# Kernel optimization log

Hardware: AMD Instinct MI355X
Metric: run time of the kernel (lower is better)

Reference implementation:

```python
import jax, jax.numpy as jnp
import numpy as np

N_NODES = 20000
N_EDGES = 150000
IN_C = 512
OUT_C = 512
K_INIT = 7  # weight has K_INIT+1 = 8 slices, all used by the forward loop


def setup_inputs() -> dict:
    key = jax.random.key(0)
    k1, k2, k3, k4 = jax.random.split(key, 4)
    x = jax.random.normal(k1, (N_NODES, IN_C), dtype=jnp.float32)
    edge_index = jax.random.randint(k2, (2, N_EDGES), 0, N_NODES, dtype=jnp.int32)
    # uniform init as in reset_parameters: bound = 1/sqrt(in_channels * (K+1))
    bound = 1.0 / np.sqrt(IN_C * (K_INIT + 1))
    weight = jax.random.uniform(k3, (K_INIT + 1, IN_C, OUT_C), dtype=jnp.float32,
                                minval=-bound, maxval=bound)
    bias = jax.random.uniform(k4, (OUT_C,), dtype=jnp.float32,
                              minval=-bound, maxval=bound)
    return {"x": x, "edge_index": edge_index, "weight": weight, "bias": bias}


def _spmm(row, col, lap, x, num_nodes):
    # out[i] = sum_{e: row[e]==i} lap[e] * x[col[e]]
    msgs = lap[:, None] * x[col]  # [E, C] gather + scale
    return jax.ops.segment_sum(msgs, row, num_segments=num_nodes)


def reference(x, edge_index, weight, bias):
    row, col = edge_index[0], edge_index[1]
    num_nodes = x.shape[0]
    Kw = weight.shape[0]
    # degree^{-1/2} normalization of implicit adjacency, edge_attr = ones
    deg = jax.ops.segment_sum(jnp.ones_like(row, dtype=x.dtype), row,
                              num_segments=num_nodes)
    dinv = jnp.where(deg > 0, jax.lax.rsqrt(jnp.maximum(deg, 1e-30)), 0.0)
    lap = -dinv[row] * dinv[col]  # [E]
    Tx_0 = x
    out = Tx_0 @ weight[0]
    Tx_1 = _spmm(row, col, lap, x, num_nodes)
    out = out + Tx_1 @ weight[1]
    for k in range(2, Kw):
        Tx_2 = 2.0 * _spmm(row, col, lap, Tx_1, num_nodes) - Tx_0
        out = out + Tx_2 @ weight[k]
        Tx_0, Tx_1 = Tx_1, Tx_2
    return out + bias
```

## Files before the change

### kernel.cpp

```cpp
#include <hip/hip_runtime.h>

#define NN 20000
#define NP 20096
#define NE 150000
#define CC 512
#define KW 8
#define KT 4096
#define SCB 20

typedef __attribute__((ext_vector_type(8))) short short8;
typedef __attribute__((ext_vector_type(4))) float f32x4;
typedef __attribute__((ext_vector_type(4))) unsigned short ushort4v;
typedef __attribute__((ext_vector_type(8))) unsigned short ushort8v;

__device__ inline unsigned short f2bf(float f) {
  unsigned u = __builtin_bit_cast(unsigned, f);
  u += 0x7fffu + ((u >> 16) & 1u);
  return (unsigned short)(u >> 16);
}

__device__ inline float bf2f(unsigned short u) {
  return __builtin_bit_cast(float, (unsigned)u << 16);
}

__device__ inline void gload_lds16(const void* g, void* l) {
  __builtin_amdgcn_global_load_lds(
      (const __attribute__((address_space(1))) unsigned int*)g,
      (__attribute__((address_space(3))) unsigned int*)l, 16, 0, 0);
}


__global__ __launch_bounds__(256) void k_zero(int* __restrict__ deg, int* __restrict__ cursor) {
  int i = blockIdx.x * blockDim.x + threadIdx.x;
  if (i < NN) { deg[i] = 0; cursor[i] = 0; }
}

__global__ __launch_bounds__(256) void k_count(const int* __restrict__ row, int* __restrict__ deg) {
  int e = blockIdx.x * blockDim.x + threadIdx.x;
  if (e < NE) atomicAdd(&deg[row[e]], 1);
}

__global__ __launch_bounds__(256) void k_dinv(const int* __restrict__ deg, float* __restrict__ dinv) {
  int i = blockIdx.x * blockDim.x + threadIdx.x;
  if (i < NN) {
    int d = deg[i];
    dinv[i] = (d > 0) ? rsqrtf((float)d) : 0.0f;
  }
}

__global__ __launch_bounds__(1024) void k_scanA(const int* __restrict__ deg,
    int* __restrict__ row_off, int* __restrict__ bsum) {
  __shared__ int sm[1024];
  const int b = blockIdx.x, tid = threadIdx.x;
  int i = b * 1024 + tid;
  int v = (i < NN) ? deg[i] : 0;
  sm[tid] = v;
  __syncthreads();
  #pragma unroll
  for (int off = 1; off < 1024; off <<= 1) {
    int t = (tid >= off) ? sm[tid - off] : 0;
    __syncthreads();
    if (tid >= off) sm[tid] += t;
    __syncthreads();
  }
  if (i < NN) row_off[i] = sm[tid] - v;
  if (tid == 1023) bsum[b] = sm[1023];
}

__global__ __launch_bounds__(64) void k_scanB(int* __restrict__ bsum) {
  if (threadIdx.x == 0) {
    int run = 0;
    for (int b = 0; b < SCB; ++b) { int t = bsum[b]; bsum[b] = run; run += t; }
  }
}

__global__ __launch_bounds__(1024) void k_scanC(int* __restrict__ row_off, const int* __restrict__ bsum) {
  int i = blockIdx.x * 1024 + threadIdx.x;
  if (i < NN) row_off[i] += bsum[blockIdx.x];
  if (i == NN - 1) row_off[NN] = NE;
}

__global__ __launch_bounds__(256) void k_fill(const int* __restrict__ row, const int* __restrict__ col,
    const int* __restrict__ row_off, int* __restrict__ cursor, const float* __restrict__ dinv,
    int* __restrict__ csr_col, float* __restrict__ csr_val) {
  int e = blockIdx.x * blockDim.x + threadIdx.x;
  if (e < NE) {
    int r = row[e], c = col[e];
    int pos = row_off[r] + atomicAdd(&cursor[r], 1);
    csr_col[pos] = c;
    csr_val[pos] = -dinv[r] * dinv[c];
  }
}


__global__ __launch_bounds__(256) void k_wcast(const float* __restrict__ W, unsigned short* __restrict__ Bt) {
  __shared__ float sm[64][68];
  const int t = blockIdx.x;
  const int s = t >> 6;
  const int rem = t & 63;
  const int kt0 = (rem >> 3) * 64;
  const int nt0 = (rem & 7) * 64;
  const float* w = W + ((size_t)s << 18);
  const int tid = threadIdx.x;
  #pragma unroll
  for (int i = 0; i < 4; ++i) {
    int f = tid + i * 256;
    int r = f >> 4;
    int c4 = f & 15;
    float4 v = *(const float4*)&w[(size_t)(kt0 + r) * CC + nt0 + c4 * 4];
    sm[r][c4 * 4 + 0] = v.x; sm[r][c4 * 4 + 1] = v.y;
    sm[r][c4 * 4 + 2] = v.z; sm[r][c4 * 4 + 3] = v.w;
  }
  __syncthreads();
  #pragma unroll
  for (int i = 0; i < 2; ++i) {
    int g = tid + i * 256;
    int nl = g >> 3;
    int k8 = (g & 7) * 8;
    ushort8v o;
    #pragma unroll
    for (int j = 0; j < 8; ++j) o[j] = f2bf(sm[k8 + j][nl]);
    *(ushort8v*)&Bt[(size_t)(nt0 + nl) * KT + s * CC + kt0 + k8] = o;
  }
}

__global__ __launch_bounds__(256) void k_xcast(const float* __restrict__ x, unsigned short* __restrict__ txall) {
  size_t t = (size_t)blockIdx.x * 256 + threadIdx.x;
  size_t idx = t * 8;
  if (idx >= (size_t)NN * CC) return;
  size_t r = idx >> 9;
  int c = (int)(idx & 511);
  const float4* p = (const float4*)&x[idx];
  float4 a = p[0], b = p[1];
  ushort8v v;
  v[0] = f2bf(a.x); v[1] = f2bf(a.y); v[2] = f2bf(a.z); v[3] = f2bf(a.w);
  v[4] = f2bf(b.x); v[5] = f2bf(b.y); v[6] = f2bf(b.z); v[7] = f2bf(b.w);
  *(ushort8v*)&txall[r * KT + c] = v;
}


__global__ __launch_bounds__(256) void k_spmm(const unsigned short* __restrict__ gsrc,
    const unsigned short* __restrict__ gprev, unsigned short* __restrict__ gdst,
    const int* __restrict__ row_off, const int* __restrict__ csr_col,
    const float* __restrict__ csr_val, float alpha, float beta)
{
  const int tid = threadIdx.x;
  const int i = blockIdx.x * 4 + (tid >> 6);
  const int c8 = (tid & 63) * 8;
  const int e0 = row_off[i];
  const int e1 = row_off[i + 1];

  float acc[8] = {};
  for (int base = e0; base < e1; base += 8) {
    int   idxs[8];
    float vals[8];
    #pragma unroll
    for (int q = 0; q < 8; ++q) {
      int ee = base + q;
      bool ok = ee < e1;
      int ec = ok ? ee : (e1 - 1);
      idxs[q] = csr_col[ec];
      vals[q] = ok ? csr_val[ec] : 0.0f;
    }
    ushort8v xs[8];
    #pragma unroll
    for (int q = 0; q < 8; ++q)
      xs[q] = *(const ushort8v*)&gsrc[(size_t)idxs[q] * KT + c8];
    #pragma unroll
    for (int q = 0; q < 8; ++q)
      #pragma unroll
      for (int p = 0; p < 8; ++p)
        acc[p] += vals[q] * bf2f(xs[q][p]);
  }

  ushort8v bv;
  if (beta != 0.0f) {
    const ushort8v p = *(const ushort8v*)&gprev[(size_t)i * KT + c8];
    #pragma unroll
    for (int q = 0; q < 8; ++q)
      bv[q] = f2bf(alpha * acc[q] + beta * bf2f(p[q]));
  } else {
    #pragma unroll
    for (int q = 0; q < 8; ++q)
      bv[q] = f2bf(alpha * acc[q]);
  }
  *(ushort8v*)&gdst[(size_t)i * KT + c8] = bv;
}


__global__ __launch_bounds__(512) void k_gemm(const unsigned short* __restrict__ A,
    const unsigned short* __restrict__ Bt, float* __restrict__ C,
    const float* __restrict__ bias)
{
  __shared__ unsigned short smA[128 * 32];
  __shared__ unsigned short smB[128 * 32];
  const int tid  = threadIdx.x;
  const int lane = tid & 63;
  const int wave = tid >> 6;
  const int wr = wave >> 2;
  const int wc = wave & 3;

  const int nwg = (NP / 128) * 4;
  int bid = blockIdx.x;
  int q = nwg >> 3, rr = nwg & 7;
  int xcd = bid & 7, lid = bid >> 3;
  int wgid = (xcd < rr ? xcd * (q + 1) : rr * (q + 1) + (xcd - rr) * q) + lid;
  const int m0 = (wgid >> 2) * 128;
  const int n0 = (wgid & 3) * 128;

  const int srow = lane >> 2;
  const int skc  = (lane & 3) * 8;

  f32x4 acc[4][2] = {};

  for (int k0 = 0; k0 < KT; k0 += 32) {
    {
      int row = wave * 16;
      gload_lds16(&A[(size_t)(m0 + row + srow) * KT + k0 + skc], &smA[row * 32]);
      gload_lds16(&Bt[(size_t)(n0 + row + srow) * KT + k0 + skc], &smB[row * 32]);
    }
    __syncthreads();

    short8 af[4], bfv[2];
    #pragma unroll
    for (int f = 0; f < 4; ++f)
      af[f]  = *(const short8*)&smA[(wr * 64 + f * 16 + (lane & 15)) * 32 + (lane >> 4) * 8];
    #pragma unroll
    for (int f = 0; f < 2; ++f)
      bfv[f] = *(const short8*)&smB[(wc * 32 + f * 16 + (lane & 15)) * 32 + (lane >> 4) * 8];
    #pragma unroll
    for (int fm = 0; fm < 4; ++fm)
      #pragma unroll
      for (int fn = 0; fn < 2; ++fn)
        acc[fm][fn] = __builtin_amdgcn_mfma_f32_16x16x32_bf16(af[fm], bfv[fn], acc[fm][fn], 0, 0, 0);
    __syncthreads();
  }

  const int prow = (lane >> 4) * 4;
  const int pcol = lane & 15;
  #pragma unroll
  for (int fm = 0; fm < 4; ++fm) {
    #pragma unroll
    for (int fn = 0; fn < 2; ++fn) {
      int gcol = n0 + wc * 32 + fn * 16 + pcol;
      float bb = bias[gcol];
      #pragma unroll
      for (int j = 0; j < 4; ++j) {
        int grow = m0 + wr * 64 + fm * 16 + prow + j;
        if (grow < NN) C[(size_t)grow * CC + gcol] = acc[fm][fn][j] + bb;
      }
    }
  }
}


extern "C" void kernel_launch(void* const* d_in, const int* in_sizes, int n_in,
                              void* d_out, int out_size, void* d_ws, size_t ws_size,
                              hipStream_t stream) {
  const float* x      = (const float*)d_in[0];
  const int*   row    = (const int*)d_in[1];
  const int*   col    = row + NE;
  const float* weight = (const float*)d_in[2];
  const float* bias   = (const float*)d_in[3];
  float* out = (float*)d_out;

  unsigned short* TxAll = (unsigned short*)d_ws;
  unsigned short* Bt    = TxAll + (size_t)NP * KT;
  float* dinv    = (float*)(Bt + (size_t)CC * KT);
  float* csr_val = dinv + NN;
  int*   deg     = (int*)(csr_val + NE);
  int*   cursor  = deg + NN;
  int*   row_off = cursor + NN;
  int*   csr_col = row_off + NN + 1;
  int*   bsum    = csr_col + NE;

  k_zero<<<(NN + 255) / 256, 256, 0, stream>>>(deg, cursor);
  k_count<<<(NE + 255) / 256, 256, 0, stream>>>(row, deg);
  k_dinv<<<(NN + 255) / 256, 256, 0, stream>>>(deg, dinv);
  k_scanA<<<SCB, 1024, 0, stream>>>(deg, row_off, bsum);
  k_scanB<<<1, 64, 0, stream>>>(bsum);
  k_scanC<<<SCB, 1024, 0, stream>>>(row_off, bsum);
  k_fill<<<(NE + 255) / 256, 256, 0, stream>>>(row, col, row_off, cursor, dinv, csr_col, csr_val);

  k_wcast<<<512, 256, 0, stream>>>(weight, Bt);
  k_xcast<<<(NN * CC / 8 + 255) / 256, 256, 0, stream>>>(x, TxAll);

  const int spmm_grid = NN / 4;
  k_spmm<<<spmm_grid, 256, 0, stream>>>(TxAll, TxAll, TxAll + CC, row_off, csr_col, csr_val, 1.0f, 0.0f);
  for (int k = 2; k < KW; ++k)
    k_spmm<<<spmm_grid, 256, 0, stream>>>(TxAll + (size_t)(k - 1) * CC, TxAll + (size_t)(k - 2) * CC,
                                          TxAll + (size_t)k * CC, row_off, csr_col, csr_val, 2.0f, -1.0f);

  k_gemm<<<(NP / 128) * 4, 512, 0, stream>>>(TxAll, Bt, out, bias);
}
```

Before: 347.2 us.

## Fuse dinv into scan, hoist spmm prev load, use 4-wave GEMM tiles

```diff
diff --git a/kernel.cpp b/kernel.cpp
--- a/kernel.cpp
+++ b/kernel.cpp
@@ -30,9 +30,9 @@
 }
 
 
-__global__ __launch_bounds__(256) void k_zero(int* __restrict__ deg, int* __restrict__ cursor) {
+__global__ __launch_bounds__(256) void k_zero(int* __restrict__ deg) {
   int i = blockIdx.x * blockDim.x + threadIdx.x;
-  if (i < NN) { deg[i] = 0; cursor[i] = 0; }
+  if (i < NN) deg[i] = 0;
 }
 
 __global__ __launch_bounds__(256) void k_count(const int* __restrict__ row, int* __restrict__ deg) {
@@ -40,20 +40,13 @@
   if (e < NE) atomicAdd(&deg[row[e]], 1);
 }
 
-__global__ __launch_bounds__(256) void k_dinv(const int* __restrict__ deg, float* __restrict__ dinv) {
-  int i = blockIdx.x * blockDim.x + threadIdx.x;
-  if (i < NN) {
-    int d = deg[i];
-    dinv[i] = (d > 0) ? rsqrtf((float)d) : 0.0f;
-  }
-}
-
 __global__ __launch_bounds__(1024) void k_scanA(const int* __restrict__ deg,
-    int* __restrict__ row_off, int* __restrict__ bsum) {
+    int* __restrict__ row_off, int* __restrict__ bsum, float* __restrict__ dinv) {
   __shared__ int sm[1024];
   const int b = blockIdx.x, tid = threadIdx.x;
   int i = b * 1024 + tid;
   int v = (i < NN) ? deg[i] : 0;
+  if (i < NN) dinv[i] = (v > 0) ? rsqrtf((float)v) : 0.0f;
   sm[tid] = v;
   __syncthreads();
   #pragma unroll
@@ -74,9 +67,10 @@
   }
 }
 
-__global__ __launch_bounds__(1024) void k_scanC(int* __restrict__ row_off, const int* __restrict__ bsum) {
+__global__ __launch_bounds__(1024) void k_scanC(int* __restrict__ row_off, const int* __restrict__ bsum,
+                                                int* __restrict__ cursor) {
   int i = blockIdx.x * 1024 + threadIdx.x;
-  if (i < NN) row_off[i] += bsum[blockIdx.x];
+  if (i < NN) { row_off[i] += bsum[blockIdx.x]; cursor[i] = 0; }
   if (i == NN - 1) row_off[NN] = NE;
 }
 
@@ -150,6 +144,9 @@
   const int e0 = row_off[i];
   const int e1 = row_off[i + 1];
 
+  ushort8v pv = {};
+  if (beta != 0.0f) pv = *(const ushort8v*)&gprev[(size_t)i * KT + c8];
+
   float acc[8] = {};
   for (int base = e0; base < e1; base += 8) {
     int   idxs[8];
@@ -175,10 +172,9 @@
 
   ushort8v bv;
   if (beta != 0.0f) {
-    const ushort8v p = *(const ushort8v*)&gprev[(size_t)i * KT + c8];
-    #pragma unroll
-    for (int q = 0; q < 8; ++q)
-      bv[q] = f2bf(alpha * acc[q] + beta * bf2f(p[q]));
+    #pragma unroll
+    for (int q = 0; q < 8; ++q)
+      bv[q] = f2bf(alpha * acc[q] + beta * bf2f(pv[q]));
   } else {
     #pragma unroll
     for (int q = 0; q < 8; ++q)
@@ -188,7 +184,7 @@
 }
 
 
-__global__ __launch_bounds__(512) void k_gemm(const unsigned short* __restrict__ A,
+__global__ __launch_bounds__(256) void k_gemm(const unsigned short* __restrict__ A,
     const unsigned short* __restrict__ Bt, float* __restrict__ C,
     const float* __restrict__ bias)
 {
@@ -197,8 +193,7 @@
   const int tid  = threadIdx.x;
   const int lane = tid & 63;
   const int wave = tid >> 6;
-  const int wr = wave >> 2;
-  const int wc = wave & 3;
+  const int wr = wave >> 1, wc = wave & 1;
 
   const int nwg = (NP / 128) * 4;
   int bid = blockIdx.x;
@@ -211,27 +206,27 @@
   const int srow = lane >> 2;
   const int skc  = (lane & 3) * 8;
 
-  f32x4 acc[4][2] = {};
+  f32x4 acc[4][4] = {};
 
   for (int k0 = 0; k0 < KT; k0 += 32) {
-    {
-      int row = wave * 16;
+    #pragma unroll
+    for (int i = 0; i < 2; ++i) {
+      int row = wave * 32 + i * 16;
       gload_lds16(&A[(size_t)(m0 + row + srow) * KT + k0 + skc], &smA[row * 32]);
       gload_lds16(&Bt[(size_t)(n0 + row + srow) * KT + k0 + skc], &smB[row * 32]);
     }
     __syncthreads();
 
-    short8 af[4], bfv[2];
-    #pragma unroll
-    for (int f = 0; f < 4; ++f)
+    short8 af[4], bfv[4];
+    #pragma unroll
+    for (int f = 0; f < 4; ++f) {
       af[f]  = *(const short8*)&smA[(wr * 64 + f * 16 + (lane & 15)) * 32 + (lane >> 4) * 8];
-    #pragma unroll
-    for (int f = 0; f < 2; ++f)
-      bfv[f] = *(const short8*)&smB[(wc * 32 + f * 16 + (lane & 15)) * 32 + (lane >> 4) * 8];
+      bfv[f] = *(const short8*)&smB[(wc * 64 + f * 16 + (lane & 15)) * 32 + (lane >> 4) * 8];
+    }
     #pragma unroll
     for (int fm = 0; fm < 4; ++fm)
       #pragma unroll
-      for (int fn = 0; fn < 2; ++fn)
+      for (int fn = 0; fn < 4; ++fn)
         acc[fm][fn] = __builtin_amdgcn_mfma_f32_16x16x32_bf16(af[fm], bfv[fn], acc[fm][fn], 0, 0, 0);
     __syncthreads();
   }
@@ -241,8 +236,8 @@
   #pragma unroll
   for (int fm = 0; fm < 4; ++fm) {
     #pragma unroll
-    for (int fn = 0; fn < 2; ++fn) {
-      int gcol = n0 + wc * 32 + fn * 16 + pcol;
+    for (int fn = 0; fn < 4; ++fn) {
+      int gcol = n0 + wc * 64 + fn * 16 + pcol;
       float bb = bias[gcol];
       #pragma unroll
       for (int j = 0; j < 4; ++j) {
@@ -274,12 +269,11 @@
   int*   csr_col = row_off + NN + 1;
   int*   bsum    = csr_col + NE;
 
-  k_zero<<<(NN + 255) / 256, 256, 0, stream>>>(deg, cursor);
+  k_zero<<<(NN + 255) / 256, 256, 0, stream>>>(deg);
   k_count<<<(NE + 255) / 256, 256, 0, stream>>>(row, deg);
-  k_dinv<<<(NN + 255) / 256, 256, 0, stream>>>(deg, dinv);
-  k_scanA<<<SCB, 1024, 0, stream>>>(deg, row_off, bsum);
+  k_scanA<<<SCB, 1024, 0, stream>>>(deg, row_off, bsum, dinv);
   k_scanB<<<1, 64, 0, stream>>>(bsum);
-  k_scanC<<<SCB, 1024, 0, stream>>>(row_off, bsum);
+  k_scanC<<<SCB, 1024, 0, stream>>>(row_off, bsum, cursor);
   k_fill<<<(NE + 255) / 256, 256, 0, stream>>>(row, col, row_off, cursor, dinv, csr_col, csr_val);
 
   k_wcast<<<512, 256, 0, stream>>>(weight, Bt);
@@ -291,5 +285,5 @@
     k_spmm<<<spmm_grid, 256, 0, stream>>>(TxAll + (size_t)(k - 1) * CC, TxAll + (size_t)(k - 2) * CC,
                                           TxAll + (size_t)k * CC, row_off, csr_col, csr_val, 2.0f, -1.0f);
 
-  k_gemm<<<(NP / 128) * 4, 512, 0, stream>>>(TxAll, Bt, out, bias);
-}
+  k_gemm<<<(NP / 128) * 4, 256, 0, stream>>>(TxAll, Bt, out, bias);
+}
```

Result: faster. 339.0 us (-2.4%).
